# Performance work log

Measured on AMD Instinct MI355X. Metric: run time of the kernel, lower is better.

## Reference

```python
import jax, jax.numpy as jnp
import numpy as np

N = 20000      # nodes
E = 160000     # edges (before self-loops)
B = 128        # graphs in batch
NEG_SLOPE = 0.2


def gat_layer(x, src, dst, W, a_src, a_dst, b):
    # x: [N, Cin]; W: [Cin, H*C]; a_src/a_dst: [H, C]; b: [C]
    H, C = a_src.shape
    n = x.shape[0]
    xw = (x @ W).reshape(n, H, C)                      # [N, H, C]
    alpha_src = jnp.sum(xw * a_src, axis=-1)           # [N, H]
    alpha_dst = jnp.sum(xw * a_dst, axis=-1)           # [N, H]
    e = jax.nn.leaky_relu(alpha_src[src] + alpha_dst[dst], NEG_SLOPE)  # [Etot, H]
    # numerically stable segment softmax over edges grouped by target node
    m = jax.ops.segment_max(e, dst, num_segments=n)    # [N, H]
    m = jnp.where(jnp.isfinite(m), m, 0.0)
    ex = jnp.exp(e - m[dst])                           # [Etot, H]
    den = jax.ops.segment_sum(ex, dst, num_segments=n) # [N, H]
    alpha = ex / (den[dst] + 1e-16)                    # [Etot, H]
    out = jax.ops.segment_sum(alpha[:, :, None] * xw[src], dst, num_segments=n)  # [N, H, C]
    return out.mean(axis=1) + b                        # concat=False -> head mean + bias


def setup_inputs() -> dict:
    key = jax.random.key(0)
    ks = jax.random.split(key, 12)
    s = 0.05
    x = jax.random.normal(ks[0], (N, 768), dtype=jnp.float32)
    edge_index = jax.random.randint(ks[1], (2, E), 0, N, dtype=jnp.int64)
    batch = jnp.sort(jax.random.randint(ks[2], (N,), 0, B, dtype=jnp.int64))
    W1 = jax.random.normal(ks[3], (768, 4 * 512), dtype=jnp.float32) * s
    a_src1 = jax.random.normal(ks[4], (4, 512), dtype=jnp.float32) * s
    a_dst1 = jax.random.normal(ks[5], (4, 512), dtype=jnp.float32) * s
    b1 = jnp.zeros((512,), dtype=jnp.float32)
    W2 = jax.random.normal(ks[6], (512, 4 * 256), dtype=jnp.float32) * s
    a_src2 = jax.random.normal(ks[7], (4, 256), dtype=jnp.float32) * s
    a_dst2 = jax.random.normal(ks[8], (4, 256), dtype=jnp.float32) * s
    b2 = jnp.zeros((256,), dtype=jnp.float32)
    fcW = jax.random.normal(ks[9], (256, 2), dtype=jnp.float32) * s
    fcb = jnp.zeros((2,), dtype=jnp.float32)
    return {"x": x, "edge_index": edge_index, "batch": batch,
            "W1": W1, "a_src1": a_src1, "a_dst1": a_dst1, "b1": b1,
            "W2": W2, "a_src2": a_src2, "a_dst2": a_dst2, "b2": b2,
            "fcW": fcW, "fcb": fcb}


def reference(x, edge_index, batch, W1, a_src1, a_dst1, b1, W2, a_src2, a_dst2, b2, fcW, fcb):
    n = x.shape[0]
    loops = jnp.arange(n, dtype=edge_index.dtype)      # GATConv adds self-loops by default
    src = jnp.concatenate([edge_index[0], loops])
    dst = jnp.concatenate([edge_index[1], loops])
    h = gat_layer(x, src, dst, W1, a_src1, a_dst1, b1)   # [N, 512]
    h = gat_layer(h, src, dst, W2, a_src2, a_dst2, b2)   # [N, 256]
    sums = jax.ops.segment_sum(h, batch, num_segments=B)                     # [B, 256]
    cnt = jax.ops.segment_sum(jnp.ones((n,), h.dtype), batch, num_segments=B)
    g = sums / jnp.maximum(cnt, 1.0)[:, None]            # scatter_mean
    return g @ fcW + fcb                                  # [B, 2]
```

## Files before the change

kernel.cpp:

```cpp
#include <hip/hip_runtime.h>

#define NN    20000
#define NE    160000
#define NETOT 180000
#define NB    128

typedef __attribute__((ext_vector_type(4))) float f32x4;
typedef __attribute__((ext_vector_type(8))) short s16x8;

__device__ __forceinline__ unsigned short f2bf(float f){
  unsigned u = __float_as_uint(f);
  return (unsigned short)((u + 0x7FFFu + ((u >> 16) & 1u)) >> 16);
}
__device__ __forceinline__ float bf2f(unsigned short h){
  return __uint_as_float(((unsigned)h) << 16);
}
__device__ __forceinline__ void gload16(const void* g, void* l){
  __builtin_amdgcn_global_load_lds((const __attribute__((address_space(1))) void*)g,
                                   (__attribute__((address_space(3))) void*)l, 16, 0, 0);
}

__global__ void k_cvt(const float* __restrict__ in, unsigned short* __restrict__ outp, int n4){
  int i = blockIdx.x * blockDim.x + threadIdx.x;
  if (i >= n4) return;
  float4 v = ((const float4*)in)[i];
  ushort4 h;
  h.x = f2bf(v.x); h.y = f2bf(v.y); h.z = f2bf(v.z); h.w = f2bf(v.w);
  ((ushort4*)outp)[i] = h;
}

__global__ void k_tcvt(const float* __restrict__ W, unsigned short* __restrict__ T, int K, int N){
  __shared__ float tile[32][33];
  int tx = threadIdx.x, ty = threadIdx.y;
  int n = blockIdx.x * 32 + tx, k = blockIdx.y * 32 + ty;
  tile[ty][tx] = W[(size_t)k * N + n];
  __syncthreads();
  int n2 = blockIdx.x * 32 + ty, k2 = blockIdx.y * 32 + tx;
  T[(size_t)n2 * K + k2] = f2bf(tile[tx][ty]);
}

__global__ __launch_bounds__(512, 2)
void gemm256(const unsigned short* __restrict__ A, const unsigned short* __restrict__ BT,
             unsigned short* __restrict__ C, int M, int N, int K, int ntile){
  __shared__ unsigned short sA[4][8192];
  __shared__ unsigned short sB[4][8192];
  const int t = threadIdx.x;
  const int lane = t & 63;
  const int w = t >> 6;
  const int wr = w >> 2, wc = w & 3;
  const int mt = blockIdx.x / ntile, nt = blockIdx.x % ntile;
  const int m0 = mt << 8, n0 = nt << 8;
  const int NK = K >> 5;

  int offA[8], offB[4];
#pragma unroll
  for (int m = 0; m < 8; ++m){
    int row = wr * 128 + m * 16 + (lane & 15);
    offA[m] = row * 32 + (((lane >> 4) ^ ((row >> 1) & 3)) << 3);
  }
#pragma unroll
  for (int n = 0; n < 4; ++n){
    int row = wc * 64 + n * 16 + (lane & 15);
    offB[n] = row * 32 + (((lane >> 4) ^ ((row >> 1) & 3)) << 3);
  }

  const int srow = t >> 2;
  const int cg8 = (((t & 3) ^ ((srow >> 1) & 3)) << 3);
  int ar0 = m0 + srow;        if (ar0 >= M) ar0 = M - 1;
  int ar1 = m0 + 128 + srow;  if (ar1 >= M) ar1 = M - 1;
  const unsigned short* apr0 = A + (size_t)ar0 * K + cg8;
  const unsigned short* apr1 = A + (size_t)ar1 * K + cg8;
  const unsigned short* bpr0 = BT + (size_t)(n0 + srow) * K + cg8;
  const unsigned short* bpr1 = BT + (size_t)(n0 + 128 + srow) * K + cg8;
  const int dst0 = srow * 32 + ((t & 3) << 3);

#define STAGE0(s) { int _b = (s) & 3; int _k = (s) << 5; \
    gload16(apr0 + _k, &sA[_b][dst0]); \
    gload16(bpr0 + _k, &sB[_b][dst0]); }
#define STAGE1(s) { int _b = (s) & 3; int _k = (s) << 5; \
    gload16(apr1 + _k, &sA[_b][dst0 + 4096]); \
    gload16(bpr1 + _k, &sB[_b][dst0 + 4096]); }

  f32x4 acc[8][4];
#pragma unroll
  for (int i = 0; i < 8; ++i)
#pragma unroll
    for (int j = 0; j < 4; ++j) acc[i][j] = (f32x4){0.f, 0.f, 0.f, 0.f};

  STAGE0(0); STAGE1(0); STAGE0(1); STAGE1(1); STAGE0(2); STAGE1(2);
  asm volatile("s_waitcnt vmcnt(8)" ::: "memory");
  __builtin_amdgcn_s_barrier();
  __builtin_amdgcn_sched_barrier(0);

  for (int ks = 0; ks < NK; ++ks){
    const int buf = ks & 3;
    const unsigned short* pa = &sA[buf][0];
    const unsigned short* pb = &sB[buf][0];
    s16x8 av[4], bv[4];
#pragma unroll
    for (int i = 0; i < 4; ++i) av[i] = *(const s16x8*)(pa + offA[i]);
#pragma unroll
    for (int i = 0; i < 4; ++i) bv[i] = *(const s16x8*)(pb + offB[i]);
    if (ks + 3 < NK) STAGE0(ks + 3);
    __builtin_amdgcn_s_barrier();
    __builtin_amdgcn_sched_barrier(0);
    __builtin_amdgcn_s_setprio(1);
#pragma unroll
    for (int mi = 0; mi < 4; ++mi)
#pragma unroll
      for (int ni = 0; ni < 4; ++ni)
        acc[mi][ni] = __builtin_amdgcn_mfma_f32_16x16x32_bf16(av[mi], bv[ni], acc[mi][ni], 0, 0, 0);
    __builtin_amdgcn_s_setprio(0);
    __builtin_amdgcn_s_barrier();
    __builtin_amdgcn_sched_barrier(0);
    s16x8 av2[4];
#pragma unroll
    for (int i = 0; i < 4; ++i) av2[i] = *(const s16x8*)(pa + offA[4 + i]);
    if (ks + 3 < NK) STAGE1(ks + 3);
    if (ks < NK - 3)      { asm volatile("s_waitcnt vmcnt(8)" ::: "memory"); }
    else if (ks == NK - 3){ asm volatile("s_waitcnt vmcnt(4)" ::: "memory"); }
    else if (ks == NK - 2){ asm volatile("s_waitcnt vmcnt(0)" ::: "memory"); }
    __builtin_amdgcn_s_barrier();
    __builtin_amdgcn_sched_barrier(0);
    __builtin_amdgcn_s_setprio(1);
#pragma unroll
    for (int mi = 0; mi < 4; ++mi)
#pragma unroll
      for (int ni = 0; ni < 4; ++ni)
        acc[4 + mi][ni] = __builtin_amdgcn_mfma_f32_16x16x32_bf16(av2[mi], bv[ni], acc[4 + mi][ni], 0, 0, 0);
    __builtin_amdgcn_s_setprio(0);
    __builtin_amdgcn_s_barrier();
    __builtin_amdgcn_sched_barrier(0);
  }
#undef STAGE0
#undef STAGE1

#pragma unroll
  for (int mi = 0; mi < 8; ++mi)
#pragma unroll
    for (int ni = 0; ni < 4; ++ni){
      int col = n0 + wc * 64 + ni * 16 + (lane & 15);
#pragma unroll
      for (int r = 0; r < 4; ++r){
        int row = m0 + wr * 128 + mi * 16 + ((lane >> 4) << 2) + r;
        if (row < M) C[(size_t)row * N + col] = f2bf(acc[mi][ni][r]);
      }
    }
}

template<int C>
__global__ void k_alpha(const unsigned short* __restrict__ xw, const float* __restrict__ a_src,
                        const float* __restrict__ a_dst, float* __restrict__ asrc,
                        float* __restrict__ adst){
  const int n = blockIdx.x, t = threadIdx.x;
  constexpr int W = C / 8;
  const int head = (t * 8) / C;
  const int c0 = (t * 8) % C;
  s16x8 v = *(const s16x8*)(xw + (size_t)n * 4 * C + t * 8);
  float4 s0 = *(const float4*)(a_src + head * C + c0);
  float4 s1 = *(const float4*)(a_src + head * C + c0 + 4);
  float4 d0 = *(const float4*)(a_dst + head * C + c0);
  float4 d1 = *(const float4*)(a_dst + head * C + c0 + 4);
  float f[8];
#pragma unroll
  for (int j = 0; j < 8; ++j) f[j] = bf2f((unsigned short)v[j]);
  float ps = f[0]*s0.x + f[1]*s0.y + f[2]*s0.z + f[3]*s0.w
           + f[4]*s1.x + f[5]*s1.y + f[6]*s1.z + f[7]*s1.w;
  float pd = f[0]*d0.x + f[1]*d0.y + f[2]*d0.z + f[3]*d0.w
           + f[4]*d1.x + f[5]*d1.y + f[6]*d1.z + f[7]*d1.w;
#pragma unroll
  for (int off = W / 2; off; off >>= 1){
    ps += __shfl_xor(ps, off);
    pd += __shfl_xor(pd, off);
  }
  if ((t & (W - 1)) == 0){
    asrc[n * 4 + head] = ps;
    adst[n * 4 + head] = pd;
  }
}

__global__ void k_count(const int* __restrict__ ei, int* __restrict__ counts){
  int e = blockIdx.x * blockDim.x + threadIdx.x;
  if (e >= NETOT) return;
  int d = (e < NE) ? ei[NE + e] : (e - NE);
  atomicAdd(&counts[d], 1);
}
__global__ void k_scan(const int* __restrict__ counts, int* __restrict__ row_ptr,
                       int* __restrict__ cursor){
  __shared__ int lds[1024];
  int t = threadIdx.x;
  int base = 0;
  for (int c0 = 0; c0 < NN; c0 += 1024){
    int i = c0 + t;
    int v = (i < NN) ? counts[i] : 0;
    __syncthreads();
    lds[t] = v;
    __syncthreads();
    for (int off = 1; off < 1024; off <<= 1){
      int x = (t >= off) ? lds[t - off] : 0;
      __syncthreads();
      lds[t] += x;
      __syncthreads();
    }
    int excl = base + lds[t] - v;
    if (i < NN){ row_ptr[i] = excl; cursor[i] = excl; }
    base += lds[1023];
  }
  if (t == 0) row_ptr[NN] = base;
}
__global__ void k_scatter(const int* __restrict__ ei, int* __restrict__ cursor,
                          int* __restrict__ csr_src){
  int e = blockIdx.x * blockDim.x + threadIdx.x;
  if (e >= NETOT) return;
  int s, d;
  if (e < NE){ s = ei[e]; d = ei[NE + e]; } else { s = d = e - NE; }
  int pos = atomicAdd(&cursor[d], 1);
  csr_src[pos] = s;
}

__global__ void k_edge(const int* __restrict__ rp, const int* __restrict__ csrc,
                       const float* __restrict__ asrc, const float* __restrict__ adst,
                       float* __restrict__ ex, float* __restrict__ den){
  int n = blockIdx.x * 4 + (threadIdx.x >> 6);
  if (n >= NN) return;
  int lane = threadIdx.x & 63;
  int beg = rp[n], end = rp[n + 1];
  float4 ad = ((const float4*)adst)[n];
  float mx0 = -1e30f, mx1 = -1e30f, mx2 = -1e30f, mx3 = -1e30f;
  for (int i = beg + lane; i < end; i += 64){
    int s = csrc[i];
    float4 as = ((const float4*)asrc)[s];
    float v0 = as.x + ad.x; v0 = v0 > 0.f ? v0 : 0.2f * v0; mx0 = fmaxf(mx0, v0);
    float v1 = as.y + ad.y; v1 = v1 > 0.f ? v1 : 0.2f * v1; mx1 = fmaxf(mx1, v1);
    float v2 = as.z + ad.z; v2 = v2 > 0.f ? v2 : 0.2f * v2; mx2 = fmaxf(mx2, v2);
    float v3 = as.w + ad.w; v3 = v3 > 0.f ? v3 : 0.2f * v3; mx3 = fmaxf(mx3, v3);
  }
#pragma unroll
  for (int off = 32; off; off >>= 1){
    mx0 = fmaxf(mx0, __shfl_xor(mx0, off));
    mx1 = fmaxf(mx1, __shfl_xor(mx1, off));
    mx2 = fmaxf(mx2, __shfl_xor(mx2, off));
    mx3 = fmaxf(mx3, __shfl_xor(mx3, off));
  }
  float s0 = 0.f, s1 = 0.f, s2 = 0.f, s3 = 0.f;
  for (int i = beg + lane; i < end; i += 64){
    int s = csrc[i];
    float4 as = ((const float4*)asrc)[s];
    float v0 = as.x + ad.x; v0 = v0 > 0.f ? v0 : 0.2f * v0;
    float v1 = as.y + ad.y; v1 = v1 > 0.f ? v1 : 0.2f * v1;
    float v2 = as.z + ad.z; v2 = v2 > 0.f ? v2 : 0.2f * v2;
    float v3 = as.w + ad.w; v3 = v3 > 0.f ? v3 : 0.2f * v3;
    float e0 = __expf(v0 - mx0), e1 = __expf(v1 - mx1);
    float e2 = __expf(v2 - mx2), e3 = __expf(v3 - mx3);
    s0 += e0; s1 += e1; s2 += e2; s3 += e3;
    ((float4*)ex)[i] = make_float4(e0, e1, e2, e3);
  }
#pragma unroll
  for (int off = 32; off; off >>= 1){
    s0 += __shfl_xor(s0, off);
    s1 += __shfl_xor(s1, off);
    s2 += __shfl_xor(s2, off);
    s3 += __shfl_xor(s3, off);
  }
  if (lane == 0) ((float4*)den)[n] = make_float4(s0, s1, s2, s3);
}

template<int C, bool BF16OUT>
__global__ void k_agg(const unsigned short* __restrict__ xw, const int* __restrict__ row_ptr,
                      const int* __restrict__ csr_src,
                      const float* __restrict__ ex, const float* __restrict__ den,
                      const float* __restrict__ bias, void* __restrict__ outp){
  const int n = blockIdx.x, t = threadIdx.x;
  float4 dv = ((const float4*)den)[n];
  float rd[4] = {1.f / (dv.x + 1e-16f), 1.f / (dv.y + 1e-16f),
                 1.f / (dv.z + 1e-16f), 1.f / (dv.w + 1e-16f)};
  float acc[4][2] = {};
  int beg = row_ptr[n], end = row_ptr[n + 1];
  for (int i = beg; i < end; ++i){
    int s = csr_src[i];
    float4 exv = ((const float4*)ex)[i];
    float al[4] = {exv.x * rd[0], exv.y * rd[1], exv.z * rd[2], exv.w * rd[3]};
    const unsigned short* sb = xw + (size_t)s * 4 * C + 2 * t;
#pragma unroll
    for (int h = 0; h < 4; ++h){
      ushort2 v = *(const ushort2*)(sb + h * C);
      acc[h][0] += al[h] * bf2f(v.x);
      acc[h][1] += al[h] * bf2f(v.y);
    }
  }
  float o0 = 0.25f * (acc[0][0] + acc[1][0] + acc[2][0] + acc[3][0]) + bias[2 * t];
  float o1 = 0.25f * (acc[0][1] + acc[1][1] + acc[2][1] + acc[3][1]) + bias[2 * t + 1];
  if (BF16OUT){
    ushort2 o; o.x = f2bf(o0); o.y = f2bf(o1);
    ((ushort2*)outp)[(size_t)n * (C / 2) + t] = o;
  } else {
    ((float2*)outp)[(size_t)n * (C / 2) + t] = make_float2(o0, o1);
  }
}

__global__ void k_pool(const float* __restrict__ h2, const int* __restrict__ batch,
                       float* __restrict__ sums, int* __restrict__ cnt){
  int n0 = blockIdx.x * 64;
  int t = threadIdx.x;
  int nend = n0 + 64; if (nend > NN) nend = NN;
  int cur = batch[n0];
  float acc = 0.f; int run = 0;
  for (int n = n0; n < nend; ++n){
    int b = batch[n];
    if (b != cur){
      atomicAdd(&sums[cur * 256 + t], acc);
      if (t == 0) atomicAdd(&cnt[cur], run);
      acc = 0.f; run = 0; cur = b;
    }
    acc += h2[(size_t)n * 256 + t];
    run++;
  }
  atomicAdd(&sums[cur * 256 + t], acc);
  if (t == 0) atomicAdd(&cnt[cur], run);
}

__global__ void k_fc(const float* __restrict__ sums, const int* __restrict__ cnt,
                     const float* __restrict__ fcW, const float* __restrict__ fcb,
                     float* __restrict__ out){
  int b = blockIdx.x, t = threadIdx.x;
  int c = cnt[b]; if (c < 1) c = 1;
  float inv = 1.f / (float)c;
  float v = sums[b * 256 + t] * inv;
  float p0 = v * fcW[t * 2];
  float p1 = v * fcW[t * 2 + 1];
#pragma unroll
  for (int off = 32; off; off >>= 1){
    p0 += __shfl_xor(p0, off);
    p1 += __shfl_xor(p1, off);
  }
  __shared__ float r0[4], r1[4];
  if ((t & 63) == 0){ r0[t >> 6] = p0; r1[t >> 6] = p1; }
  __syncthreads();
  if (t == 0){
    out[b * 2 + 0] = r0[0] + r0[1] + r0[2] + r0[3] + fcb[0];
    out[b * 2 + 1] = r1[0] + r1[1] + r1[2] + r1[3] + fcb[1];
  }
}

extern "C" void kernel_launch(void* const* d_in, const int* in_sizes, int n_in,
                              void* d_out, int out_size, void* d_ws, size_t ws_size,
                              hipStream_t stream){
  const float* x      = (const float*)d_in[0];
  const int*   ei     = (const int*)d_in[1];
  const int*   batch  = (const int*)d_in[2];
  const float* W1     = (const float*)d_in[3];
  const float* a_src1 = (const float*)d_in[4];
  const float* a_dst1 = (const float*)d_in[5];
  const float* b1     = (const float*)d_in[6];
  const float* W2     = (const float*)d_in[7];
  const float* a_src2 = (const float*)d_in[8];
  const float* a_dst2 = (const float*)d_in[9];
  const float* b2     = (const float*)d_in[10];
  const float* fcW    = (const float*)d_in[11];
  const float* fcb    = (const float*)d_in[12];
  float* out = (float*)d_out;
  (void)in_sizes; (void)n_in; (void)out_size; (void)ws_size;

  char* ws = (char*)d_ws;
  size_t off = 0;
  auto take = [&](size_t bytes) -> char* {
    char* p = ws + off;
    off += (bytes + 255) & ~(size_t)255;
    return p;
  };
  char* slab0 = take(81920000);
  unsigned short* xw1 = (unsigned short*)slab0;
  unsigned short* xw2 = (unsigned short*)slab0;
  unsigned short* x_bf  = (unsigned short*)take(30720000);
  unsigned short* h1_bf = (unsigned short*)take(20480000);
  float*          h2    = (float*)take(20480000);
  unsigned short* W1T = (unsigned short*)take(3145728);
  unsigned short* W2T = (unsigned short*)take(1048576);
  float* asrc   = (float*)take(320000);
  float* adst   = (float*)take(320000);
  float* den    = (float*)take(320000);
  float* ex     = (float*)take((size_t)NETOT * 16);
  int* counts   = (int*)take(80004);
  int* row_ptr  = (int*)take(80004);
  int* cursor   = (int*)take(80004);
  int* csr_src  = (int*)take(720000);
  float* sums   = (float*)take(131072);
  int* cnt      = (int*)take(512);

  const int egrid = (NETOT + 255) / 256;

  hipMemsetAsync(counts, 0, NN * 4, stream);
  k_count<<<egrid, 256, 0, stream>>>(ei, counts);
  k_scan<<<1, 1024, 0, stream>>>(counts, row_ptr, cursor);
  k_scatter<<<egrid, 256, 0, stream>>>(ei, cursor, csr_src);

  k_cvt<<<(3840000 + 255) / 256, 256, 0, stream>>>(x, x_bf, 3840000);
  k_tcvt<<<dim3(2048 / 32, 768 / 32), dim3(32, 32), 0, stream>>>(W1, W1T, 768, 2048);
  gemm256<<<79 * 8, 512, 0, stream>>>(x_bf, W1T, xw1, NN, 2048, 768, 8);
  k_alpha<512><<<NN, 256, 0, stream>>>(xw1, a_src1, a_dst1, asrc, adst);
  k_edge<<<(NN + 3) / 4, 256, 0, stream>>>(row_ptr, csr_src, asrc, adst, ex, den);
  k_agg<512, true><<<NN, 256, 0, stream>>>(xw1, row_ptr, csr_src, ex, den, b1, h1_bf);

  k_tcvt<<<dim3(1024 / 32, 512 / 32), dim3(32, 32), 0, stream>>>(W2, W2T, 512, 1024);
  gemm256<<<79 * 4, 512, 0, stream>>>(h1_bf, W2T, xw2, NN, 1024, 512, 4);
  k_alpha<256><<<NN, 128, 0, stream>>>(xw2, a_src2, a_dst2, asrc, adst);
  k_edge<<<(NN + 3) / 4, 256, 0, stream>>>(row_ptr, csr_src, asrc, adst, ex, den);
  k_agg<256, false><<<NN, 128, 0, stream>>>(xw2, row_ptr, csr_src, ex, den, b2, h2);

  hipMemsetAsync(sums, 0, 131072, stream);
  hipMemsetAsync(cnt, 0, 512, stream);
  k_pool<<<(NN + 63) / 64, 256, 0, stream>>>(h2, batch, sums, cnt);
  k_fc<<<NB, 256, 0, stream>>>(sums, cnt, fcW, fcb, out);
}
```

Before: 548.8 us.

## Retile GEMM to 128x256 with double buffering, LDS-staged stores, and per-head aggregation

New measurement: 540.2 us. About the same (-1.6%).

```diff
diff --git a/kernel.cpp b/kernel.cpp
--- a/kernel.cpp
+++ b/kernel.cpp
@@ -39,113 +39,116 @@
   T[(size_t)n2 * K + k2] = f2bf(tile[tx][ty]);
 }
 
-__global__ __launch_bounds__(512, 2)
-void gemm256(const unsigned short* __restrict__ A, const unsigned short* __restrict__ BT,
-             unsigned short* __restrict__ C, int M, int N, int K, int ntile){
-  __shared__ unsigned short sA[4][8192];
-  __shared__ unsigned short sB[4][8192];
+__global__ __launch_bounds__(256, 2)
+void gemm_bf16(const unsigned short* __restrict__ A, const unsigned short* __restrict__ BT,
+               unsigned short* __restrict__ C, int M, int N, int K, int ntile){
+  __shared__ unsigned short lds[24576];
   const int t = threadIdx.x;
   const int lane = t & 63;
   const int w = t >> 6;
-  const int wr = w >> 2, wc = w & 3;
+  const int wr = w >> 1, wc = w & 1;
   const int mt = blockIdx.x / ntile, nt = blockIdx.x % ntile;
-  const int m0 = mt << 8, n0 = nt << 8;
+  const int m0 = mt << 7, n0 = nt << 8;
   const int NK = K >> 5;
 
-  int offA[8], offB[4];
-#pragma unroll
-  for (int m = 0; m < 8; ++m){
-    int row = wr * 128 + m * 16 + (lane & 15);
-    offA[m] = row * 32 + (((lane >> 4) ^ ((row >> 1) & 3)) << 3);
-  }
-#pragma unroll
-  for (int n = 0; n < 4; ++n){
-    int row = wc * 64 + n * 16 + (lane & 15);
-    offB[n] = row * 32 + (((lane >> 4) ^ ((row >> 1) & 3)) << 3);
-  }
-
-  const int srow = t >> 2;
-  const int cg8 = (((t & 3) ^ ((srow >> 1) & 3)) << 3);
-  int ar0 = m0 + srow;        if (ar0 >= M) ar0 = M - 1;
-  int ar1 = m0 + 128 + srow;  if (ar1 >= M) ar1 = M - 1;
-  const unsigned short* apr0 = A + (size_t)ar0 * K + cg8;
-  const unsigned short* apr1 = A + (size_t)ar1 * K + cg8;
-  const unsigned short* bpr0 = BT + (size_t)(n0 + srow) * K + cg8;
-  const unsigned short* bpr1 = BT + (size_t)(n0 + 128 + srow) * K + cg8;
-  const int dst0 = srow * 32 + ((t & 3) << 3);
-
-#define STAGE0(s) { int _b = (s) & 3; int _k = (s) << 5; \
-    gload16(apr0 + _k, &sA[_b][dst0]); \
-    gload16(bpr0 + _k, &sB[_b][dst0]); }
-#define STAGE1(s) { int _b = (s) & 3; int _k = (s) << 5; \
-    gload16(apr1 + _k, &sA[_b][dst0 + 4096]); \
-    gload16(bpr1 + _k, &sB[_b][dst0 + 4096]); }
-
-  f32x4 acc[8][4];
-#pragma unroll
-  for (int i = 0; i < 8; ++i)
-#pragma unroll
-    for (int j = 0; j < 4; ++j) acc[i][j] = (f32x4){0.f, 0.f, 0.f, 0.f};
-
-  STAGE0(0); STAGE1(0); STAGE0(1); STAGE1(1); STAGE0(2); STAGE1(2);
-  asm volatile("s_waitcnt vmcnt(8)" ::: "memory");
+  int offA[4], offB[8];
+#pragma unroll
+  for (int mi = 0; mi < 4; ++mi){
+    int row = wr * 64 + mi * 16 + (lane & 15);
+    offA[mi] = row * 32 + (((lane >> 4) ^ ((row >> 1) & 3)) << 3);
+  }
+#pragma unroll
+  for (int ni = 0; ni < 8; ++ni){
+    int row = wc * 128 + ni * 16 + (lane & 15);
+    offB[ni] = 4096 + row * 32 + (((lane >> 4) ^ ((row >> 1) & 3)) << 3);
+  }
+
+  const unsigned short* srcA[2]; int dstA[2];
+#pragma unroll
+  for (int j = 0; j < 2; ++j){
+    int rA = w * 32 + j * 16 + (lane >> 2);
+    int gr = m0 + rA; if (gr >= M) gr = M - 1;
+    srcA[j] = A + (size_t)gr * K + (((lane & 3) ^ ((rA >> 1) & 3)) << 3);
+    dstA[j] = w * 1024 + j * 512 + lane * 8;
+  }
+  const unsigned short* srcB[4]; int dstB[4];
+#pragma unroll
+  for (int j = 0; j < 4; ++j){
+    int rB = w * 64 + j * 16 + (lane >> 2);
+    srcB[j] = BT + (size_t)(n0 + rB) * K + (((lane & 3) ^ ((rB >> 1) & 3)) << 3);
+    dstB[j] = 4096 + w * 2048 + j * 512 + lane * 8;
+  }
+
+#define STAGE(ks, bo) { int _k = (ks) << 5; \
+    gload16(srcA[0] + _k, &lds[(bo) + dstA[0]]); \
+    gload16(srcA[1] + _k, &lds[(bo) + dstA[1]]); \
+    gload16(srcB[0] + _k, &lds[(bo) + dstB[0]]); \
+    gload16(srcB[1] + _k, &lds[(bo) + dstB[1]]); \
+    gload16(srcB[2] + _k, &lds[(bo) + dstB[2]]); \
+    gload16(srcB[3] + _k, &lds[(bo) + dstB[3]]); }
+
+  f32x4 acc[4][8];
+#pragma unroll
+  for (int i = 0; i < 4; ++i)
+#pragma unroll
+    for (int j = 0; j < 8; ++j) acc[i][j] = (f32x4){0.f, 0.f, 0.f, 0.f};
+
+  STAGE(0, 0);
+  asm volatile("s_waitcnt vmcnt(0)" ::: "memory");
+  __builtin_amdgcn_sched_barrier(0);
   __builtin_amdgcn_s_barrier();
   __builtin_amdgcn_sched_barrier(0);
 
   for (int ks = 0; ks < NK; ++ks){
-    const int buf = ks & 3;
-    const unsigned short* pa = &sA[buf][0];
-    const unsigned short* pb = &sB[buf][0];
-    s16x8 av[4], bv[4];
-#pragma unroll
-    for (int i = 0; i < 4; ++i) av[i] = *(const s16x8*)(pa + offA[i]);
-#pragma unroll
-    for (int i = 0; i < 4; ++i) bv[i] = *(const s16x8*)(pb + offB[i]);
-    if (ks + 3 < NK) STAGE0(ks + 3);
+    const int bo = (ks & 1) * 12288;
+    s16x8 av[4], bv[8];
+#pragma unroll
+    for (int i = 0; i < 4; ++i) av[i] = *(const s16x8*)&lds[bo + offA[i]];
+#pragma unroll
+    for (int i = 0; i < 8; ++i) bv[i] = *(const s16x8*)&lds[bo + offB[i]];
+    if (ks + 1 < NK) STAGE(ks + 1, 12288 - bo);
+    __builtin_amdgcn_s_setprio(1);
+#pragma unroll
+    for (int mi = 0; mi < 4; ++mi)
+#pragma unroll
+      for (int ni = 0; ni < 8; ++ni)
+        acc[mi][ni] = __builtin_amdgcn_mfma_f32_16x16x32_bf16(av[mi], bv[ni], acc[mi][ni], 0, 0, 0);
+    __builtin_amdgcn_s_setprio(0);
+    asm volatile("s_waitcnt vmcnt(0)" ::: "memory");
+    __builtin_amdgcn_sched_barrier(0);
     __builtin_amdgcn_s_barrier();
     __builtin_amdgcn_sched_barrier(0);
-    __builtin_amdgcn_s_setprio(1);
-#pragma unroll
-    for (int mi = 0; mi < 4; ++mi)
-#pragma unroll
-      for (int ni = 0; ni < 4; ++ni)
-        acc[mi][ni] = __builtin_amdgcn_mfma_f32_16x16x32_bf16(av[mi], bv[ni], acc[mi][ni], 0, 0, 0);
-    __builtin_amdgcn_s_setprio(0);
-    __builtin_amdgcn_s_barrier();
-    __builtin_amdgcn_sched_barrier(0);
-    s16x8 av2[4];
-#pragma unroll
-    for (int i = 0; i < 4; ++i) av2[i] = *(const s16x8*)(pa + offA[4 + i]);
-    if (ks + 3 < NK) STAGE1(ks + 3);
-    if (ks < NK - 3)      { asm volatile("s_waitcnt vmcnt(8)" ::: "memory"); }
-    else if (ks == NK - 3){ asm volatile("s_waitcnt vmcnt(4)" ::: "memory"); }
-    else if (ks == NK - 2){ asm volatile("s_waitcnt vmcnt(0)" ::: "memory"); }
-    __builtin_amdgcn_s_barrier();
-    __builtin_amdgcn_sched_barrier(0);
-    __builtin_amdgcn_s_setprio(1);
-#pragma unroll
-    for (int mi = 0; mi < 4; ++mi)
-#pragma unroll
-      for (int ni = 0; ni < 4; ++ni)
-        acc[4 + mi][ni] = __builtin_amdgcn_mfma_f32_16x16x32_bf16(av2[mi], bv[ni], acc[4 + mi][ni], 0, 0, 0);
-    __builtin_amdgcn_s_setprio(0);
-    __builtin_amdgcn_s_barrier();
-    __builtin_amdgcn_sched_barrier(0);
-  }
-#undef STAGE0
-#undef STAGE1
-
-#pragma unroll
-  for (int mi = 0; mi < 8; ++mi)
-#pragma unroll
-    for (int ni = 0; ni < 4; ++ni){
-      int col = n0 + wc * 64 + ni * 16 + (lane & 15);
-#pragma unroll
-      for (int r = 0; r < 4; ++r){
-        int row = m0 + wr * 128 + mi * 16 + ((lane >> 4) << 2) + r;
-        if (row < M) C[(size_t)row * N + col] = f2bf(acc[mi][ni][r]);
-      }
+  }
+#undef STAGE
+
+#pragma unroll
+  for (int h = 0; h < 2; ++h){
+    if (wr == h){
+#pragma unroll
+      for (int mi = 0; mi < 4; ++mi)
+#pragma unroll
+        for (int ni = 0; ni < 8; ++ni)
+#pragma unroll
+          for (int r = 0; r < 4; ++r){
+            int rl = mi * 16 + ((lane >> 4) << 2) + r;
+            int col = wc * 128 + ni * 16 + (lane & 15);
+            int byte = (rl * 512 + col * 2) ^ (((rl >> 2) & 3) << 5);
+            *(unsigned short*)((char*)lds + byte) = f2bf(acc[mi][ni][r]);
+          }
     }
+    __syncthreads();
+#pragma unroll
+    for (int it = 0; it < 8; ++it){
+      int idx = it * 256 + t;
+      int rl = idx >> 5, c16 = idx & 31;
+      int byte = (rl * 512 + c16 * 16) ^ (((rl >> 2) & 3) << 5);
+      s16x8 v = *(const s16x8*)((const char*)lds + byte);
+      int grow = m0 + h * 64 + rl;
+      if (grow < M)
+        *(s16x8*)(C + (size_t)grow * N + n0 + c16 * 8) = v;
+    }
+    __syncthreads();
+  }
 }
 
 template<int C>
@@ -271,30 +274,40 @@
                       const float* __restrict__ ex, const float* __restrict__ den,
                       const float* __restrict__ bias, void* __restrict__ outp){
   const int n = blockIdx.x, t = threadIdx.x;
-  float4 dv = ((const float4*)den)[n];
-  float rd[4] = {1.f / (dv.x + 1e-16f), 1.f / (dv.y + 1e-16f),
-                 1.f / (dv.z + 1e-16f), 1.f / (dv.w + 1e-16f)};
-  float acc[4][2] = {};
+  constexpr int LPH = C / 8;
+  const int h = t / LPH, c0 = (t % LPH) * 8;
+  __shared__ float red[4][C];
+  float rdh = 1.f / (den[n * 4 + h] + 1e-16f);
+  float acc[8] = {};
   int beg = row_ptr[n], end = row_ptr[n + 1];
+  const unsigned short* xwh = xw + h * C + c0;
   for (int i = beg; i < end; ++i){
     int s = csr_src[i];
-    float4 exv = ((const float4*)ex)[i];
-    float al[4] = {exv.x * rd[0], exv.y * rd[1], exv.z * rd[2], exv.w * rd[3]};
-    const unsigned short* sb = xw + (size_t)s * 4 * C + 2 * t;
-#pragma unroll
-    for (int h = 0; h < 4; ++h){
-      ushort2 v = *(const ushort2*)(sb + h * C);
-      acc[h][0] += al[h] * bf2f(v.x);
-      acc[h][1] += al[h] * bf2f(v.y);
+    float aa = ex[i * 4 + h] * rdh;
+    s16x8 v = *(const s16x8*)(xwh + (size_t)s * 4 * C);
+#pragma unroll
+    for (int j = 0; j < 8; ++j) acc[j] += aa * bf2f((unsigned short)v[j]);
+  }
+#pragma unroll
+  for (int j = 0; j < 8; ++j) red[h][c0 + j] = acc[j];
+  __syncthreads();
+  if (t < LPH){
+    int cc = t * 8;
+    float o[8];
+#pragma unroll
+    for (int j = 0; j < 8; ++j)
+      o[j] = 0.25f * (red[0][cc + j] + red[1][cc + j] + red[2][cc + j] + red[3][cc + j])
+           + bias[cc + j];
+    if (BF16OUT){
+      union { unsigned short u[8]; s16x8 v; } pk;
+#pragma unroll
+      for (int j = 0; j < 8; ++j) pk.u[j] = f2bf(o[j]);
+      *(s16x8*)((unsigned short*)outp + (size_t)n * C + cc) = pk.v;
+    } else {
+      float* op = (float*)outp + (size_t)n * C + cc;
+      ((float4*)op)[0] = make_float4(o[0], o[1], o[2], o[3]);
+      ((float4*)op)[1] = make_float4(o[4], o[5], o[6], o[7]);
     }
-  }
-  float o0 = 0.25f * (acc[0][0] + acc[1][0] + acc[2][0] + acc[3][0]) + bias[2 * t];
-  float o1 = 0.25f * (acc[0][1] + acc[1][1] + acc[2][1] + acc[3][1]) + bias[2 * t + 1];
-  if (BF16OUT){
-    ushort2 o; o.x = f2bf(o0); o.y = f2bf(o1);
-    ((ushort2*)outp)[(size_t)n * (C / 2) + t] = o;
-  } else {
-    ((float2*)outp)[(size_t)n * (C / 2) + t] = make_float2(o0, o1);
   }
 }
 
@@ -396,13 +409,13 @@
 
   k_cvt<<<(3840000 + 255) / 256, 256, 0, stream>>>(x, x_bf, 3840000);
   k_tcvt<<<dim3(2048 / 32, 768 / 32), dim3(32, 32), 0, stream>>>(W1, W1T, 768, 2048);
-  gemm256<<<79 * 8, 512, 0, stream>>>(x_bf, W1T, xw1, NN, 2048, 768, 8);
+  gemm_bf16<<<157 * 8, 256, 0, stream>>>(x_bf, W1T, xw1, NN, 2048, 768, 8);
   k_alpha<512><<<NN, 256, 0, stream>>>(xw1, a_src1, a_dst1, asrc, adst);
   k_edge<<<(NN + 3) / 4, 256, 0, stream>>>(row_ptr, csr_src, asrc, adst, ex, den);
   k_agg<512, true><<<NN, 256, 0, stream>>>(xw1, row_ptr, csr_src, ex, den, b1, h1_bf);
 
   k_tcvt<<<dim3(1024 / 32, 512 / 32), dim3(32, 32), 0, stream>>>(W2, W2T, 512, 1024);
-  gemm256<<<79 * 4, 512, 0, stream>>>(h1_bf, W2T, xw2, NN, 1024, 512, 4);
+  gemm_bf16<<<157 * 4, 256, 0, stream>>>(h1_bf, W2T, xw2, NN, 1024, 512, 4);
   k_alpha<256><<<NN, 128, 0, stream>>>(xw2, a_src2, a_dst2, asrc, adst);
   k_edge<<<(NN + 3) / 4, 256, 0, stream>>>(row_ptr, csr_src, asrc, adst, ex, den);
   k_agg<256, false><<<NN, 128, 0, stream>>>(xw2, row_ptr, csr_src, ex, den, b2, h2);
```
